# Kernel optimization log

Measured on AMD Instinct MI355X. Metric: run time of the kernel, lower is better.

The kernel has to match this reference:

```python
import jax, jax.numpy as jnp
import numpy as np

N_JOINTS = 50
N_BONES = 50  # mask slicing [:, :, :50] / [:, :, :150] in the source requires exactly 50 bones
# Original repo's getSkeletalModelStructure() is not provided; use deterministic
# bone pairs (i, (i+1) % 50) over the 50 joints. Same gather+norm+direction math.
BONE_A = np.arange(N_JOINTS)
BONE_B = (BONE_A + 1) % N_JOINTS


def _length_direct(x):
    # x: [B, T, 150] -> joints [B, T, 50, 3]
    B, T, _ = x.shape
    joints = x.reshape(B, T, N_JOINTS, 3)
    diff = joints[:, :, BONE_A, :] - joints[:, :, BONE_B, :]  # [B, T, 50, 3]
    length = jnp.linalg.norm(diff, axis=-1)                   # [B, T, 50]
    tiny = jnp.finfo(x.dtype).tiny
    direct = diff / (length[..., None] + tiny)                # [B, T, 50, 3]
    return length, direct.reshape(B, T, N_BONES * 3)          # [B, T, 150]


def setup_inputs() -> dict:
    key = jax.random.key(0)
    k1, k2 = jax.random.split(key)
    shape = (128, 1024, 150)
    return {
        "preds": jax.random.normal(k1, shape, dtype=jnp.float32),
        "targets": jax.random.normal(k2, shape, dtype=jnp.float32),
    }


def reference(preds, targets):
    target_pad = 0.0
    loss_scale = 0.1
    mask = (targets != target_pad).astype(preds.dtype)  # [B, T, 150]
    p = preds * mask
    t = targets * mask
    # lengths are computed in the original but unused in the final loss;
    # only the direction terms enter the bone loss.
    _, p_dir = _length_direct(p)
    _, t_dir = _length_direct(t)
    p_dir = p_dir * mask[:, :, :150]
    t_dir = t_dir * mask[:, :, :150]
    loss = jnp.mean(jnp.abs(p - t)) + 0.1 * jnp.mean((p_dir - t_dir) ** 2)
    return loss * loss_scale
```

## Files before the change

### kernel.cpp

```cpp
#include <hip/hip_runtime.h>

constexpr int   FRAMES   = 128 * 1024;
constexpr int   NB       = 50;
constexpr int   FRAME_F  = 150;
constexpr float SCALE    = 0.1f / (float)(FRAMES * FRAME_F);

constexpr int FPW    = 16;
constexpr int NWAVES = FRAMES / FPW;
constexpr int BLOCK  = 256;
constexpr int NBLK   = NWAVES * 64 / BLOCK;

__global__ __launch_bounds__(256) void bone_loss_main(
    const float* __restrict__ preds,
    const float* __restrict__ targets,
    float* __restrict__ partials)
{
    const int gid   = blockIdx.x * BLOCK + threadIdx.x;
    const int wave  = gid >> 6;
    const int lane  = threadIdx.x & 63;
    const bool act  = lane < NB;
    const int  jcl  = act ? lane : (NB - 1);
    const int  sidx = (lane >= NB - 1) ? lane - (NB - 1) : lane + 1;

    const long fbase = (long)wave * FPW;
    const float* pp = preds   + fbase * FRAME_F + jcl * 3;
    const float* tp = targets + fbase * FRAME_F + jcl * 3;

    float acc = 0.0f;

    float p0 = pp[0], p1 = pp[1], p2 = pp[2];
    float t0 = tp[0], t1 = tp[1], t2 = tp[2];

    #pragma unroll
    for (int i = 0; i < FPW; ++i) {
        float np0 = 0.f, np1 = 0.f, np2 = 0.f, nt0 = 0.f, nt1 = 0.f, nt2 = 0.f;
        if (i + 1 < FPW) {
            const float* npp = pp + (i + 1) * FRAME_F;
            const float* ntp = tp + (i + 1) * FRAME_F;
            np0 = npp[0]; np1 = npp[1]; np2 = npp[2];
            nt0 = ntp[0]; nt1 = ntp[1]; nt2 = ntp[2];
        }

        const float m0 = (t0 != 0.0f) ? 1.0f : 0.0f;
        const float m1 = (t1 != 0.0f) ? 1.0f : 0.0f;
        const float m2 = (t2 != 0.0f) ? 1.0f : 0.0f;
        const float pm0 = p0 * m0, pm1 = p1 * m1, pm2 = p2 * m2;

        const float ab = fabsf(pm0 - t0) + fabsf(pm1 - t1) + fabsf(pm2 - t2);

        const float qm0 = __shfl(pm0, sidx, 64);
        const float qm1 = __shfl(pm1, sidx, 64);
        const float qm2 = __shfl(pm2, sidx, 64);
        const float u0  = __shfl(t0,  sidx, 64);
        const float u1  = __shfl(t1,  sidx, 64);
        const float u2  = __shfl(t2,  sidx, 64);

        const float pd0 = pm0 - qm0, pd1 = pm1 - qm1, pd2 = pm2 - qm2;
        const float td0 = t0  - u0,  td1 = t1  - u1,  td2 = t2  - u2;

        const float pl2 = pd0*pd0 + pd1*pd1 + pd2*pd2;
        const float tl2 = td0*td0 + td1*td1 + td2*td2;
        const float pri = (pl2 > 0.0f) ? __builtin_amdgcn_rsqf(pl2) : 0.0f;
        const float tri = (tl2 > 0.0f) ? __builtin_amdgcn_rsqf(tl2) : 0.0f;

        const float d0 = pd0 * pri - td0 * tri;
        const float d1 = pd1 * pri - td1 * tri;
        const float d2 = pd2 * pri - td2 * tri;
        const float sq = m0*d0*d0 + m1*d1*d1 + m2*d2*d2;

        acc += act ? (ab + 0.1f * sq) : 0.0f;

        p0 = np0; p1 = np1; p2 = np2;
        t0 = nt0; t1 = nt1; t2 = nt2;
    }

    #pragma unroll
    for (int off = 32; off > 0; off >>= 1)
        acc += __shfl_down(acc, off, 64);

    __shared__ float ws[4];
    const int wid = threadIdx.x >> 6;
    if ((threadIdx.x & 63) == 0) ws[wid] = acc;
    __syncthreads();
    if (threadIdx.x == 0)
        partials[blockIdx.x] = ws[0] + ws[1] + ws[2] + ws[3];
}

__global__ __launch_bounds__(256) void bone_loss_finish(
    const float* __restrict__ partials,
    float* __restrict__ out)
{
    float v = 0.0f;
    for (int i = threadIdx.x; i < NBLK; i += 256)
        v += partials[i];

    #pragma unroll
    for (int off = 32; off > 0; off >>= 1)
        v += __shfl_down(v, off, 64);

    __shared__ float ws[4];
    const int wid = threadIdx.x >> 6;
    if ((threadIdx.x & 63) == 0) ws[wid] = v;
    __syncthreads();
    if (threadIdx.x == 0)
        out[0] = (ws[0] + ws[1] + ws[2] + ws[3]) * SCALE;
}

extern "C" void kernel_launch(void* const* d_in, const int* in_sizes, int n_in,
                              void* d_out, int out_size, void* d_ws, size_t ws_size,
                              hipStream_t stream) {
    const float* preds   = (const float*)d_in[0];
    const float* targets = (const float*)d_in[1];
    float* out      = (float*)d_out;
    float* partials = (float*)d_ws;

    bone_loss_main<<<NBLK, BLOCK, 0, stream>>>(preds, targets, partials);
    bone_loss_finish<<<1, 256, 0, stream>>>(partials, out);
}
```

Measured before the change: 174.4 us.

## Map threads to flat joint indices with grid-stride loop instead of per-wave frames

Replaces the one-wave-per-16-frames layout (64 lanes with only 50 active, neighbour joint fetched by shuffle) with a flat mapping where every thread handles one joint per iteration across a fixed 2048-block grid-stride loop. The neighbouring joint is loaded directly from memory, with the wraparound offset computed arithmetically from the stride pattern. This removes the idle lanes and the cross-lane shuffles and makes loads contiguous across all lanes. In exchange each element is loaded twice (own joint and neighbour, mostly cache hits), the mask is computed twice, and the grid is smaller with launch_bounds occupancy hints.

```diff
diff --git a/kernel.cpp b/kernel.cpp
--- a/kernel.cpp
+++ b/kernel.cpp
@@ -1,77 +1,81 @@
 #include <hip/hip_runtime.h>
 
-constexpr int   FRAMES   = 128 * 1024;
-constexpr int   NB       = 50;
-constexpr int   FRAME_F  = 150;
-constexpr float SCALE    = 0.1f / (float)(FRAMES * FRAME_F);
+constexpr int      FRAMES  = 128 * 1024;
+constexpr int      FRAME_F = 150;
+constexpr unsigned NT      = (unsigned)FRAMES * 50u;
+constexpr float    SCALE   = 0.1f / ((float)FRAMES * (float)FRAME_F);
 
-constexpr int FPW    = 16;
-constexpr int NWAVES = FRAMES / FPW;
-constexpr int BLOCK  = 256;
-constexpr int NBLK   = NWAVES * 64 / BLOCK;
+constexpr int      BLOCK   = 256;
+constexpr int      NBLK    = 2048;
+constexpr unsigned STRIDE  = (unsigned)BLOCK * NBLK;
+constexpr int      FULL    = NT / STRIDE;
 
-__global__ __launch_bounds__(256) void bone_loss_main(
+__device__ __forceinline__ float bone_term(const float* __restrict__ ps,
+                                           const float* __restrict__ ts,
+                                           int no)
+{
+    const float* pn = ps + no;
+    const float* tn = ts + no;
+
+    const float p0 = ps[0], p1 = ps[1], p2 = ps[2];
+    const float t0 = ts[0], t1 = ts[1], t2 = ts[2];
+    const float q0 = pn[0], q1 = pn[1], q2 = pn[2];
+    const float u0 = tn[0], u1 = tn[1], u2 = tn[2];
+
+    const float m0 = (t0 != 0.0f) ? 1.0f : 0.0f;
+    const float m1 = (t1 != 0.0f) ? 1.0f : 0.0f;
+    const float m2 = (t2 != 0.0f) ? 1.0f : 0.0f;
+    const float n0 = (u0 != 0.0f) ? 1.0f : 0.0f;
+    const float n1 = (u1 != 0.0f) ? 1.0f : 0.0f;
+    const float n2 = (u2 != 0.0f) ? 1.0f : 0.0f;
+
+    const float pm0 = p0 * m0, pm1 = p1 * m1, pm2 = p2 * m2;
+    const float qm0 = q0 * n0, qm1 = q1 * n1, qm2 = q2 * n2;
+
+    const float ab = fabsf(pm0 - t0) + fabsf(pm1 - t1) + fabsf(pm2 - t2);
+
+    const float pd0 = pm0 - qm0, pd1 = pm1 - qm1, pd2 = pm2 - qm2;
+    const float td0 = t0 - u0,   td1 = t1 - u1,   td2 = t2 - u2;
+
+    const float pl2 = pd0*pd0 + pd1*pd1 + pd2*pd2;
+    const float tl2 = td0*td0 + td1*td1 + td2*td2;
+    const float pri = (pl2 > 0.0f) ? __builtin_amdgcn_rsqf(pl2) : 0.0f;
+    const float tri = (tl2 > 0.0f) ? __builtin_amdgcn_rsqf(tl2) : 0.0f;
+
+    const float d0 = pd0 * pri - td0 * tri;
+    const float d1 = pd1 * pri - td1 * tri;
+    const float d2 = pd2 * pri - td2 * tri;
+    const float sq = m0*d0*d0 + m1*d1*d1 + m2*d2*d2;
+
+    return ab + 0.1f * sq;
+}
+
+__global__ __launch_bounds__(BLOCK, 4) void bone_loss_main(
     const float* __restrict__ preds,
     const float* __restrict__ targets,
     float* __restrict__ partials)
 {
-    const int gid   = blockIdx.x * BLOCK + threadIdx.x;
-    const int wave  = gid >> 6;
-    const int lane  = threadIdx.x & 63;
-    const bool act  = lane < NB;
-    const int  jcl  = act ? lane : (NB - 1);
-    const int  sidx = (lane >= NB - 1) ? lane - (NB - 1) : lane + 1;
-
-    const long fbase = (long)wave * FPW;
-    const float* pp = preds   + fbase * FRAME_F + jcl * 3;
-    const float* tp = targets + fbase * FRAME_F + jcl * 3;
+    const unsigned g  = blockIdx.x * BLOCK + threadIdx.x;
+    const unsigned j0 = g % 50u;
 
     float acc = 0.0f;
 
-    float p0 = pp[0], p1 = pp[1], p2 = pp[2];
-    float t0 = tp[0], t1 = tp[1], t2 = tp[2];
+    #pragma unroll
+    for (int b = 0; b < FULL; ++b) {
+        const unsigned kb  = 49u - (38u * (unsigned)b) % 50u;
+        const int      no  = (j0 == kb) ? (3 - FRAME_F) : 3;
+        const size_t   e   = (size_t)(g + (unsigned)b * STRIDE) * 3u;
+        acc += bone_term(preds + e, targets + e, no);
+    }
 
-    #pragma unroll
-    for (int i = 0; i < FPW; ++i) {
-        float np0 = 0.f, np1 = 0.f, np2 = 0.f, nt0 = 0.f, nt1 = 0.f, nt2 = 0.f;
-        if (i + 1 < FPW) {
-            const float* npp = pp + (i + 1) * FRAME_F;
-            const float* ntp = tp + (i + 1) * FRAME_F;
-            np0 = npp[0]; np1 = npp[1]; np2 = npp[2];
-            nt0 = ntp[0]; nt1 = ntp[1]; nt2 = ntp[2];
+    {
+        const unsigned idx = g + (unsigned)FULL * STRIDE;
+        if (idx < NT) {
+            const unsigned kb = 49u - (38u * (unsigned)FULL) % 50u;
+            const int      no = (j0 == kb) ? (3 - FRAME_F) : 3;
+            const size_t   e  = (size_t)idx * 3u;
+            acc += bone_term(preds + e, targets + e, no);
         }
-
-        const float m0 = (t0 != 0.0f) ? 1.0f : 0.0f;
-        const float m1 = (t1 != 0.0f) ? 1.0f : 0.0f;
-        const float m2 = (t2 != 0.0f) ? 1.0f : 0.0f;
-        const float pm0 = p0 * m0, pm1 = p1 * m1, pm2 = p2 * m2;
-
-        const float ab = fabsf(pm0 - t0) + fabsf(pm1 - t1) + fabsf(pm2 - t2);
-
-        const float qm0 = __shfl(pm0, sidx, 64);
-        const float qm1 = __shfl(pm1, sidx, 64);
-        const float qm2 = __shfl(pm2, sidx, 64);
-        const float u0  = __shfl(t0,  sidx, 64);
-        const float u1  = __shfl(t1,  sidx, 64);
-        const float u2  = __shfl(t2,  sidx, 64);
-
-        const float pd0 = pm0 - qm0, pd1 = pm1 - qm1, pd2 = pm2 - qm2;
-        const float td0 = t0  - u0,  td1 = t1  - u1,  td2 = t2  - u2;
-
-        const float pl2 = pd0*pd0 + pd1*pd1 + pd2*pd2;
-        const float tl2 = td0*td0 + td1*td1 + td2*td2;
-        const float pri = (pl2 > 0.0f) ? __builtin_amdgcn_rsqf(pl2) : 0.0f;
-        const float tri = (tl2 > 0.0f) ? __builtin_amdgcn_rsqf(tl2) : 0.0f;
-
-        const float d0 = pd0 * pri - td0 * tri;
-        const float d1 = pd1 * pri - td1 * tri;
-        const float d2 = pd2 * pri - td2 * tri;
-        const float sq = m0*d0*d0 + m1*d1*d1 + m2*d2*d2;
-
-        acc += act ? (ab + 0.1f * sq) : 0.0f;
-
-        p0 = np0; p1 = np1; p2 = np2;
-        t0 = nt0; t1 = nt1; t2 = nt2;
     }
 
     #pragma unroll
```

Result: slower. 178.0 us (+2.1%).
